# Kernel optimization log

Measured on AMD Instinct MI355X. Metric: run time of the kernel, lower is better.

Reference implementation:

```python
import jax, jax.numpy as jnp
import numpy as np

EPS_LN = 1e-5

def layer_norm(x, g, b):
    mu = x.mean(-1, keepdims=True)
    var = ((x - mu) ** 2).mean(-1, keepdims=True)
    return (x - mu) / jnp.sqrt(var + EPS_LN) * g + b

def spike(x):
    # MultiSpike: quantized spike activation, forward = clip(round(x), 0, 4)
    return jnp.clip(jnp.round(x), 0.0, 4.0)

def setup_inputs() -> dict:
    key = jax.random.key(0)
    ks = jax.random.split(key, 8)
    B, C, H, W = 16, 256, 56, 56
    hid = 128
    inp = {}
    inp['feature_map'] = jax.random.normal(ks[0], (B, C, H, W), jnp.float32)
    inp['audio_feature'] = jax.random.normal(ks[1], (B, 1, C), jnp.float32)
    # MINE params
    inp['w1'] = jax.random.normal(ks[2], (hid, 2 * C), jnp.float32) / np.sqrt(2 * C)
    inp['b1'] = jnp.zeros((hid,), jnp.float32)
    inp['g1'] = jnp.ones((hid,), jnp.float32)
    inp['beta1'] = jnp.zeros((hid,), jnp.float32)
    inp['w2'] = jax.random.normal(ks[3], (hid // 2, hid), jnp.float32) / np.sqrt(hid)
    inp['b2'] = jnp.zeros((hid // 2,), jnp.float32)
    inp['g2'] = jnp.ones((hid // 2,), jnp.float32)
    inp['beta2'] = jnp.zeros((hid // 2,), jnp.float32)
    inp['w3'] = jax.random.normal(ks[4], (1, hid // 2), jnp.float32) / np.sqrt(hid // 2)
    inp['b3'] = jnp.zeros((1,), jnp.float32)
    # MI params
    inp['pw'] = jax.random.normal(ks[5], (C, C), jnp.float32) / np.sqrt(C)
    inp['pb'] = jnp.zeros((C,), jnp.float32)
    inp['pg'] = jnp.ones((C,), jnp.float32)
    inp['pbeta'] = jnp.zeros((C,), jnp.float32)
    return inp

def reference(feature_map, audio_feature, w1, b1, g1, beta1, w2, b2, g2, beta2,
              w3, b3, pw, pb, pg, pbeta):
    B, C, H, W = feature_map.shape
    # visual tokens: [B*H*W, C]
    visual = feature_map.transpose(0, 2, 3, 1).reshape(B * H * W, C)
    # broadcast audio to every spatial position: [B*H*W, C]
    audio = jnp.broadcast_to(audio_feature[:, 0][:, None, None, :], (B, H, W, C)).reshape(B * H * W, C)
    # MINE MLP on joint features
    joint = jnp.concatenate([visual, audio], axis=1)            # [BHW, 2C]
    h = spike(layer_norm(joint @ w1.T + b1, g1, beta1))          # [BHW, 128]
    h = spike(layer_norm(h @ w2.T + b2, g2, beta2))              # [BHW, 64]
    mi = (h @ w3.T + b3)[:, 0]                                   # [BHW]
    mi_map = mi.reshape(B, 1, H * W)
    fm_flat = feature_map.reshape(B, C, H * W)
    # MI-weighted pooling: [B,1,C]
    x = jnp.einsum('bos,bcs->boc', mi_map, fm_flat)
    x = x @ pw.T + pb                                            # proj (dropout = eval identity)
    x = spike(layer_norm(x, pg, pbeta))                          # [B,1,C]
    fusion_map = jnp.einsum('bchw,bc->bchw', feature_map, x[:, 0])
    mi4 = mi_map.reshape(B, 1, H, W)
    mi4 = (mi4 - mi4.min()) / (mi4.max() - mi4.min() + 1e-6)     # global min-max norm
    return fusion_map, mi4
```

## Files before the change

kernel.cpp:

```cpp
#include <hip/hip_runtime.h>

#define HW 3136
#define NPOS 12845056

__device__ __forceinline__ unsigned fkey(float f) {
  unsigned u = __float_as_uint(f);
  return (u & 0x80000000u) ? ~u : (u | 0x80000000u);
}
__device__ __forceinline__ float funkey(unsigned u) {
  return __uint_as_float((u & 0x80000000u) ? (u & 0x7FFFFFFFu) : ~u);
}
__device__ __forceinline__ float spikef(float x) {
  return fminf(fmaxf(rintf(x), 0.0f), 4.0f);
}
__device__ __forceinline__ float rdlane(float v, int src) {
  return __int_as_float(__builtin_amdgcn_readlane(__float_as_int(v), src));
}

__global__ __launch_bounds__(256) void prep_kernel(
    const float* __restrict__ audio, const float* __restrict__ w1,
    const float* __restrict__ b1, const float* __restrict__ w2,
    float* __restrict__ a_pre, float* __restrict__ w1t,
    float* __restrict__ w2t, float* __restrict__ pool,
    unsigned* __restrict__ mm)
{
  __shared__ float au[256];
  const int bx = blockIdx.x, t = threadIdx.x;
  if (bx < 128) {
    int idx = bx * 256 + t;
    int c = idx >> 7, j = idx & 127;
    w1t[idx] = w1[j * 512 + c];
  } else if (bx < 160) {
    int idx = (bx - 128) * 256 + t;
    int k = idx >> 6, j2 = idx & 63;
    w2t[idx] = w2[j2 * 128 + k];
  } else if (bx < 176) {
    int b = bx - 160;
    au[t] = audio[b * 256 + t];
    __syncthreads();
    int w = t >> 6, l = t & 63;
    float a0 = au[l], a1 = au[l + 64], a2 = au[l + 128], a3 = au[l + 192];
    for (int jj = 0; jj < 32; ++jj) {
      int j = w * 32 + jj;
      const float* row = w1 + j * 512 + 256;
      float s = row[l] * a0 + row[l + 64] * a1 + row[l + 128] * a2 + row[l + 192] * a3;
      #pragma unroll
      for (int off = 32; off; off >>= 1) s += __shfl_xor(s, off);
      if (l == 0) a_pre[b * 128 + j] = s + b1[j];
    }
  } else {
    for (int i = t; i < 4096; i += 256) pool[i] = 0.0f;
    if (t == 0) { mm[0] = 0xFFFFFFFFu; mm[1] = 0u; }
  }
}

__global__ __launch_bounds__(256, 6) void mlp_kernel(
    const float* __restrict__ fm, const float* __restrict__ w1t,
    const float* __restrict__ w2t, const float* __restrict__ b2,
    const float* __restrict__ w3, const float* __restrict__ b3,
    const float* __restrict__ g1, const float* __restrict__ be1,
    const float* __restrict__ g2, const float* __restrict__ be2,
    const float* __restrict__ a_pre, float* __restrict__ mi_out,
    float* __restrict__ pool, unsigned* __restrict__ mm)
{
  __shared__ float miL[32];

  const int b  = blockIdx.y;
  const int p0 = blockIdx.x * 32;
  const int t  = threadIdx.x;
  const int l  = t & 63;
  const int wv = __builtin_amdgcn_readfirstlane(t >> 6);
  const int pos0 = p0 + wv * 8;
  const int j0 = 2 * l;

  float acc0[8], acc1[8];
  #pragma unroll
  for (int p = 0; p < 8; ++p) { acc0[p] = 0.f; acc1[p] = 0.f; }
  {
    const float* xrow = fm + (size_t)b * 256 * HW + pos0;
    const float* wrow = w1t + j0;
    #pragma unroll 4
    for (int k = 0; k < 256; ++k) {
      float4 xa = *(const float4*)(xrow + (size_t)k * HW);
      float4 xb = *(const float4*)(xrow + (size_t)k * HW + 4);
      float2 w = *(const float2*)(wrow + k * 128);
      acc0[0] = fmaf(xa.x, w.x, acc0[0]); acc1[0] = fmaf(xa.x, w.y, acc1[0]);
      acc0[1] = fmaf(xa.y, w.x, acc0[1]); acc1[1] = fmaf(xa.y, w.y, acc1[1]);
      acc0[2] = fmaf(xa.z, w.x, acc0[2]); acc1[2] = fmaf(xa.z, w.y, acc1[2]);
      acc0[3] = fmaf(xa.w, w.x, acc0[3]); acc1[3] = fmaf(xa.w, w.y, acc1[3]);
      acc0[4] = fmaf(xb.x, w.x, acc0[4]); acc1[4] = fmaf(xb.x, w.y, acc1[4]);
      acc0[5] = fmaf(xb.y, w.x, acc0[5]); acc1[5] = fmaf(xb.y, w.y, acc1[5]);
      acc0[6] = fmaf(xb.z, w.x, acc0[6]); acc1[6] = fmaf(xb.z, w.y, acc1[6]);
      acc0[7] = fmaf(xb.w, w.x, acc0[7]); acc1[7] = fmaf(xb.w, w.y, acc1[7]);
    }
  }
  {
    float2 ap = *(const float2*)(a_pre + b * 128 + j0);
    #pragma unroll
    for (int p = 0; p < 8; ++p) { acc0[p] += ap.x; acc1[p] += ap.y; }
  }

  float mu_[8];
  #pragma unroll
  for (int p = 0; p < 8; ++p) {
    float s = acc0[p] + acc1[p];
    #pragma unroll
    for (int off = 32; off; off >>= 1) s += __shfl_xor(s, off);
    mu_[p] = s * (1.0f/128.0f);
  }
  float h1a[8], h1b[8];
  {
    float2 gv = *(const float2*)(g1 + j0);
    float2 bv = *(const float2*)(be1 + j0);
    #pragma unroll
    for (int p = 0; p < 8; ++p) {
      float d0 = acc0[p] - mu_[p], d1 = acc1[p] - mu_[p];
      float s2 = d0 * d0 + d1 * d1;
      #pragma unroll
      for (int off = 32; off; off >>= 1) s2 += __shfl_xor(s2, off);
      float inv = 1.0f / sqrtf(s2 * (1.0f/128.0f) + 1e-5f);
      h1a[p] = spikef(d0 * inv * gv.x + bv.x);
      h1b[p] = spikef(d1 * inv * gv.y + bv.y);
    }
  }

  float acc2[8];
  #pragma unroll
  for (int p = 0; p < 8; ++p) acc2[p] = 0.f;
  {
    const float* w2base = w2t + l;
    #pragma unroll 2
    for (int kp = 0; kp < 64; ++kp) {
      float wA = w2base[(2*kp) * 64];
      float wB = w2base[(2*kp+1) * 64];
      #pragma unroll
      for (int p = 0; p < 8; ++p) {
        float xA = rdlane(h1a[p], kp);
        float xB = rdlane(h1b[p], kp);
        acc2[p] = fmaf(xB, wB, fmaf(xA, wA, acc2[p]));
      }
    }
  }

  const float b2l = b2[l];
  #pragma unroll
  for (int p = 0; p < 8; ++p) acc2[p] += b2l;
  float miv[8];
  {
    const float g2l = g2[l], be2l = be2[l], w3l = w3[l];
    const float b3v = b3[0];
    #pragma unroll
    for (int p = 0; p < 8; ++p) {
      float s = acc2[p];
      #pragma unroll
      for (int off = 32; off; off >>= 1) s += __shfl_xor(s, off);
      float mu2 = s * (1.0f/64.0f);
      float d = acc2[p] - mu2;
      float s2 = d * d;
      #pragma unroll
      for (int off = 32; off; off >>= 1) s2 += __shfl_xor(s2, off);
      float inv2 = 1.0f / sqrtf(s2 * (1.0f/64.0f) + 1e-5f);
      float sp = spikef(d * inv2 * g2l + be2l) * w3l;
      #pragma unroll
      for (int off = 32; off; off >>= 1) sp += __shfl_xor(sp, off);
      miv[p] = sp + b3v;
    }
  }

  {
    float m = 0.f;
    #pragma unroll
    for (int p = 0; p < 8; ++p) m = (l == p) ? miv[p] : m;
    if (l < 8) {
      mi_out[b * HW + pos0 + l] = m;
      miL[wv * 8 + l] = m;
    }
  }
  __syncthreads();

  if (wv == 0) {
    float v = miL[l & 31];
    float mn = v, mx = v;
    #pragma unroll
    for (int off = 16; off; off >>= 1) {
      mn = fminf(mn, __shfl_xor(mn, off));
      mx = fmaxf(mx, __shfl_xor(mx, off));
    }
    if (l == 0) {
      unsigned kmn = fkey(mn), kmx = fkey(mx);
      volatile unsigned* vmm = (volatile unsigned*)mm;
      if (kmn < vmm[0]) atomicMin(&mm[0], kmn);
      if (kmx > vmm[1]) atomicMax(&mm[1], kmx);
    }
  }

  {
    const int pos = l & 31, ph = l >> 5;
    const float mval = miL[pos];
    const float* fp = fm + ((size_t)(b * 256 + wv * 64 + ph * 32)) * HW + p0 + pos;
    #pragma unroll 4
    for (int ci = 0; ci < 32; ++ci) {
      float v = fp[(size_t)ci * HW] * mval;
      #pragma unroll
      for (int off = 16; off; off >>= 1) v += __shfl_xor(v, off);
      if (pos == 0) atomicAdd(&pool[b * 256 + wv * 64 + ph * 32 + ci], v);
    }
  }
}

__global__ __launch_bounds__(256) void scale_kernel(
    const float* __restrict__ pool, const float* __restrict__ pw,
    const float* __restrict__ pb, const float* __restrict__ pg,
    const float* __restrict__ pbeta, float* __restrict__ scale,
    const unsigned* __restrict__ mm, float* __restrict__ gpar)
{
  __shared__ float pl[256];
  __shared__ float xsh[256];
  __shared__ float rs[4], rs2[4];
  int b = blockIdx.x, t = threadIdx.x;
  pl[t] = pool[b*256 + t];
  __syncthreads();
  int w = t >> 6, l = t & 63;
  float p0 = pl[l], p1 = pl[l+64], p2 = pl[l+128], p3 = pl[l+192];
  for (int jj = 0; jj < 64; ++jj) {
    int j = w*64 + jj;
    const float* row = pw + j*256;
    float s = row[l]*p0 + row[l+64]*p1 + row[l+128]*p2 + row[l+192]*p3;
    #pragma unroll
    for (int off = 32; off; off >>= 1) s += __shfl_xor(s, off);
    if (l == 0) xsh[j] = s;
  }
  __syncthreads();
  float x = xsh[t] + pb[t];
  float s = x;
  #pragma unroll
  for (int off = 32; off; off >>= 1) s += __shfl_xor(s, off);
  if (l == 0) rs[w] = s;
  __syncthreads();
  float mu = (rs[0]+rs[1]+rs[2]+rs[3]) * (1.0f/256.0f);
  float d = x - mu;
  float s2 = d*d;
  #pragma unroll
  for (int off = 32; off; off >>= 1) s2 += __shfl_xor(s2, off);
  if (l == 0) rs2[w] = s2;
  __syncthreads();
  float var = (rs2[0]+rs2[1]+rs2[2]+rs2[3]) * (1.0f/256.0f);
  float v = d / sqrtf(var + 1e-5f) * pg[t] + pbeta[t];
  scale[b*256 + t] = spikef(v);
  if (b == 0 && t == 0) {
    float mn = funkey(mm[0]), mx = funkey(mm[1]);
    gpar[0] = mn;
    gpar[1] = mx - mn + 1e-6f;
  }
}

__global__ __launch_bounds__(256) void fuse_kernel(
    const float4* __restrict__ fm4, const float* __restrict__ scale,
    const float4* __restrict__ mi4, const float* __restrict__ gpar,
    float4* __restrict__ out4, float4* __restrict__ mi4out)
{
  const int c = blockIdx.x, b = blockIdx.y, t = threadIdx.x;
  if (c < 256) {
    float s = scale[b * 256 + c];
    size_t base = ((size_t)b * 256 + c) * 784;
    #pragma unroll
    for (int i = 0; i < 3; ++i) {
      int idx = t + i * 256;
      float4 v = fm4[base + idx];
      out4[base + idx] = make_float4(v.x*s, v.y*s, v.z*s, v.w*s);
    }
    int idx = t + 768;
    if (idx < 784) {
      float4 v = fm4[base + idx];
      out4[base + idx] = make_float4(v.x*s, v.y*s, v.z*s, v.w*s);
    }
  } else {
    float gmin = gpar[0], den = gpar[1];
    size_t base = (size_t)b * 784;
    #pragma unroll
    for (int i = 0; i < 3; ++i) {
      int idx = t + i * 256;
      float4 v = mi4[base + idx];
      mi4out[base + idx] = make_float4((v.x-gmin)/den, (v.y-gmin)/den,
                                       (v.z-gmin)/den, (v.w-gmin)/den);
    }
    int idx = t + 768;
    if (idx < 784) {
      float4 v = mi4[base + idx];
      mi4out[base + idx] = make_float4((v.x-gmin)/den, (v.y-gmin)/den,
                                       (v.z-gmin)/den, (v.w-gmin)/den);
    }
  }
}

extern "C" void kernel_launch(void* const* d_in, const int* in_sizes, int n_in,
                              void* d_out, int out_size, void* d_ws, size_t ws_size,
                              hipStream_t stream)
{
  const float* fm    = (const float*)d_in[0];
  const float* audio = (const float*)d_in[1];
  const float* w1    = (const float*)d_in[2];
  const float* b1    = (const float*)d_in[3];
  const float* g1    = (const float*)d_in[4];
  const float* be1   = (const float*)d_in[5];
  const float* w2    = (const float*)d_in[6];
  const float* b2    = (const float*)d_in[7];
  const float* g2    = (const float*)d_in[8];
  const float* be2   = (const float*)d_in[9];
  const float* w3    = (const float*)d_in[10];
  const float* b3    = (const float*)d_in[11];
  const float* pw    = (const float*)d_in[12];
  const float* pb    = (const float*)d_in[13];
  const float* pg    = (const float*)d_in[14];
  const float* pbeta = (const float*)d_in[15];

  float* ws    = (float*)d_ws;
  float* a_pre = ws;
  float* pool  = ws + 2048;
  float* scale = ws + 6144;
  float* mi    = ws + 10240;
  float* w1t   = ws + 60416;
  float* w2t   = ws + 93184;
  unsigned* mm = (unsigned*)(ws + 101376);
  float* gpar  = ws + 101378;

  float* out    = (float*)d_out;
  float* mi4out = out + NPOS;

  prep_kernel<<<177, 256, 0, stream>>>(audio, w1, b1, w2, a_pre, w1t, w2t,
                                       pool, mm);
  mlp_kernel<<<dim3(98, 16), 256, 0, stream>>>(fm, w1t, w2t, b2, w3, b3,
                                               g1, be1, g2, be2,
                                               a_pre, mi, pool, mm);
  scale_kernel<<<16, 256, 0, stream>>>(pool, pw, pb, pg, pbeta, scale, mm, gpar);
  fuse_kernel<<<dim3(257, 16), 256, 0, stream>>>((const float4*)fm, scale,
                                                 (const float4*)mi, gpar,
                                                 (float4*)out, (float4*)mi4out);
}
```

Baseline: 325.3 us.

## Keep each wave's feature tile in registers and reuse it for pooling

Each wave now loads its 8-position by 256-channel feature slice into 32 registers per lane at the start, and broadcasts the values to the first-layer FMAs with readlane instead of issuing repeated float4 global loads. The same register tile is reused for the MI-weighted pooling, which removes the second pass over the feature map, the shared-memory staging and the block barrier. Min/max is now reduced per wave, so there are more atomics. The cost is much higher register pressure: the occupancy hint drops from 6 to 4 and the 256-step loop is fully unrolled, and the pooling atomics are now issued per wave.

Result: slower. 424.6 us (+30.5%).

```diff
diff --git a/kernel.cpp b/kernel.cpp
--- a/kernel.cpp
+++ b/kernel.cpp
@@ -54,7 +54,7 @@
   }
 }
 
-__global__ __launch_bounds__(256, 6) void mlp_kernel(
+__global__ __launch_bounds__(256, 4) void mlp_kernel(
     const float* __restrict__ fm, const float* __restrict__ w1t,
     const float* __restrict__ w2t, const float* __restrict__ b2,
     const float* __restrict__ w3, const float* __restrict__ b3,
@@ -63,35 +63,35 @@
     const float* __restrict__ a_pre, float* __restrict__ mi_out,
     float* __restrict__ pool, unsigned* __restrict__ mm)
 {
-  __shared__ float miL[32];
-
   const int b  = blockIdx.y;
-  const int p0 = blockIdx.x * 32;
   const int t  = threadIdx.x;
   const int l  = t & 63;
   const int wv = __builtin_amdgcn_readfirstlane(t >> 6);
-  const int pos0 = p0 + wv * 8;
+  const int pos0 = blockIdx.x * 32 + wv * 8;
   const int j0 = 2 * l;
 
+  const float* fmb = fm + (size_t)b * 256 * HW + pos0;
+  const int kr = l >> 3, pp = l & 7;
+  float xr[32];
+  #pragma unroll
+  for (int r = 0; r < 32; ++r)
+    xr[r] = fmb[(size_t)(r * 8 + kr) * HW + pp];
+
   float acc0[8], acc1[8];
   #pragma unroll
   for (int p = 0; p < 8; ++p) { acc0[p] = 0.f; acc1[p] = 0.f; }
   {
-    const float* xrow = fm + (size_t)b * 256 * HW + pos0;
-    const float* wrow = w1t + j0;
-    #pragma unroll 4
+    const float* w1p = w1t + j0;
+    #pragma unroll
     for (int k = 0; k < 256; ++k) {
-      float4 xa = *(const float4*)(xrow + (size_t)k * HW);
-      float4 xb = *(const float4*)(xrow + (size_t)k * HW + 4);
-      float2 w = *(const float2*)(wrow + k * 128);
-      acc0[0] = fmaf(xa.x, w.x, acc0[0]); acc1[0] = fmaf(xa.x, w.y, acc1[0]);
-      acc0[1] = fmaf(xa.y, w.x, acc0[1]); acc1[1] = fmaf(xa.y, w.y, acc1[1]);
-      acc0[2] = fmaf(xa.z, w.x, acc0[2]); acc1[2] = fmaf(xa.z, w.y, acc1[2]);
-      acc0[3] = fmaf(xa.w, w.x, acc0[3]); acc1[3] = fmaf(xa.w, w.y, acc1[3]);
-      acc0[4] = fmaf(xb.x, w.x, acc0[4]); acc1[4] = fmaf(xb.x, w.y, acc1[4]);
-      acc0[5] = fmaf(xb.y, w.x, acc0[5]); acc1[5] = fmaf(xb.y, w.y, acc1[5]);
-      acc0[6] = fmaf(xb.z, w.x, acc0[6]); acc1[6] = fmaf(xb.z, w.y, acc1[6]);
-      acc0[7] = fmaf(xb.w, w.x, acc0[7]); acc1[7] = fmaf(xb.w, w.y, acc1[7]);
+      float2 w = *(const float2*)(w1p + (size_t)k * 128);
+      const int r = k >> 3, g = (k & 7) << 3;
+      #pragma unroll
+      for (int p = 0; p < 8; ++p) {
+        float x = rdlane(xr[r], g + p);
+        acc0[p] = fmaf(x, w.x, acc0[p]);
+        acc1[p] = fmaf(x, w.y, acc1[p]);
+      }
     }
   }
   {
@@ -124,38 +124,38 @@
     }
   }
 
-  float acc2[8];
-  #pragma unroll
-  for (int p = 0; p < 8; ++p) acc2[p] = 0.f;
-  {
-    const float* w2base = w2t + l;
-    #pragma unroll 2
-    for (int kp = 0; kp < 64; ++kp) {
-      float wA = w2base[(2*kp) * 64];
-      float wB = w2base[(2*kp+1) * 64];
+  float a2[8];
+  #pragma unroll
+  for (int p = 0; p < 8; ++p) a2[p] = 0.f;
+  {
+    const float* w2p = w2t + l;
+    #pragma unroll
+    for (int m = 0; m < 64; ++m) {
+      float wA = w2p[(2 * m) * 64];
+      float wB = w2p[(2 * m + 1) * 64];
       #pragma unroll
       for (int p = 0; p < 8; ++p) {
-        float xA = rdlane(h1a[p], kp);
-        float xB = rdlane(h1b[p], kp);
-        acc2[p] = fmaf(xB, wB, fmaf(xA, wA, acc2[p]));
+        float xA = rdlane(h1a[p], m);
+        float xB = rdlane(h1b[p], m);
+        a2[p] = fmaf(xB, wB, fmaf(xA, wA, a2[p]));
       }
     }
   }
 
   const float b2l = b2[l];
   #pragma unroll
-  for (int p = 0; p < 8; ++p) acc2[p] += b2l;
+  for (int p = 0; p < 8; ++p) a2[p] += b2l;
   float miv[8];
   {
     const float g2l = g2[l], be2l = be2[l], w3l = w3[l];
     const float b3v = b3[0];
     #pragma unroll
     for (int p = 0; p < 8; ++p) {
-      float s = acc2[p];
+      float s = a2[p];
       #pragma unroll
       for (int off = 32; off; off >>= 1) s += __shfl_xor(s, off);
       float mu2 = s * (1.0f/64.0f);
-      float d = acc2[p] - mu2;
+      float d = a2[p] - mu2;
       float s2 = d * d;
       #pragma unroll
       for (int off = 32; off; off >>= 1) s2 += __shfl_xor(s2, off);
@@ -167,25 +167,15 @@
     }
   }
 
-  {
-    float m = 0.f;
-    #pragma unroll
-    for (int p = 0; p < 8; ++p) m = (l == p) ? miv[p] : m;
-    if (l < 8) {
-      mi_out[b * HW + pos0 + l] = m;
-      miL[wv * 8 + l] = m;
-    }
-  }
-  __syncthreads();
-
-  if (wv == 0) {
-    float v = miL[l & 31];
-    float mn = v, mx = v;
-    #pragma unroll
-    for (int off = 16; off; off >>= 1) {
-      mn = fminf(mn, __shfl_xor(mn, off));
-      mx = fmaxf(mx, __shfl_xor(mx, off));
-    }
+  float m_l = miv[0];
+  #pragma unroll
+  for (int p = 1; p < 8; ++p) m_l = (pp == p) ? miv[p] : m_l;
+  if (l < 8) mi_out[b * HW + pos0 + l] = m_l;
+
+  {
+    float mn = miv[0], mx = miv[0];
+    #pragma unroll
+    for (int p = 1; p < 8; ++p) { mn = fminf(mn, miv[p]); mx = fmaxf(mx, miv[p]); }
     if (l == 0) {
       unsigned kmn = fkey(mn), kmx = fkey(mx);
       volatile unsigned* vmm = (volatile unsigned*)mm;
@@ -194,17 +184,13 @@
     }
   }
 
-  {
-    const int pos = l & 31, ph = l >> 5;
-    const float mval = miL[pos];
-    const float* fp = fm + ((size_t)(b * 256 + wv * 64 + ph * 32)) * HW + p0 + pos;
-    #pragma unroll 4
-    for (int ci = 0; ci < 32; ++ci) {
-      float v = fp[(size_t)ci * HW] * mval;
-      #pragma unroll
-      for (int off = 16; off; off >>= 1) v += __shfl_xor(v, off);
-      if (pos == 0) atomicAdd(&pool[b * 256 + wv * 64 + ph * 32 + ci], v);
-    }
+  #pragma unroll
+  for (int r = 0; r < 32; ++r) {
+    float v = xr[r] * m_l;
+    v += __shfl_xor(v, 1);
+    v += __shfl_xor(v, 2);
+    v += __shfl_xor(v, 4);
+    if (pp == 0) atomicAdd(&pool[b * 256 + r * 8 + kr], v);
   }
 }
 
```
